# Kernel tuning notes

Measured on AMD Instinct MI355X. Metric: run time of the kernel, lower is better.

## Reference

```python
import jax, jax.numpy as jnp
import numpy as np

N = 50000
E = 800000
F_IN = 128
HID = 128
N_CLS = 32


def setup_inputs() -> dict:
    key = jax.random.key(0)
    ks = jax.random.split(key, 8)
    x = jax.random.normal(ks[0], (N, F_IN), dtype=jnp.float32)
    edge_index = jax.random.randint(ks[1], (2, E), 0, N, dtype=jnp.int32)
    batch = jnp.zeros((N,), dtype=jnp.int32)
    # GCNConv learned params (glorot-ish scale)
    W1 = jax.random.normal(ks[2], (F_IN, HID), dtype=jnp.float32) / np.sqrt(F_IN)
    b1 = jnp.zeros((HID,), dtype=jnp.float32)
    W2 = jax.random.normal(ks[3], (HID, HID), dtype=jnp.float32) / np.sqrt(HID)
    b2 = jnp.zeros((HID,), dtype=jnp.float32)
    W3 = jax.random.normal(ks[4], (HID, N_CLS), dtype=jnp.float32) / np.sqrt(HID)
    b3 = jnp.zeros((N_CLS,), dtype=jnp.float32)
    return {"x": x, "edge_index": edge_index, "batch": batch,
            "W1": W1, "b1": b1, "W2": W2, "b2": b2, "W3": W3, "b3": b3}


def _gcn_norm(edge_index, num_nodes):
    """Add self-loops and compute symmetric D^-1/2 (A+I) D^-1/2 edge weights."""
    loop = jnp.arange(num_nodes, dtype=edge_index.dtype)
    row = jnp.concatenate([edge_index[0], loop])  # source
    col = jnp.concatenate([edge_index[1], loop])  # destination
    ones = jnp.ones(row.shape[0], dtype=jnp.float32)
    deg = jax.ops.segment_sum(ones, col, num_segments=num_nodes)
    dinv = jnp.where(deg > 0, jax.lax.rsqrt(deg), 0.0)
    norm = dinv[row] * dinv[col]  # [E + N]
    return row, col, norm


def _gcn_conv(x, row, col, norm, W, b):
    h = x @ W                               # [N, out]
    msg = h[row] * norm[:, None]            # gather + scale, [E+N, out]
    out = jax.ops.segment_sum(msg, col, num_segments=x.shape[0])
    return out + b


def reference(x, edge_index, batch, W1, b1, W2, b2, W3, b3):
    # eval mode: dropout(p=0.2) is identity
    num_nodes = x.shape[0]
    row, col, norm = _gcn_norm(edge_index, num_nodes)
    h = jax.nn.relu(_gcn_conv(x, row, col, norm, W1, b1))
    h = jax.nn.relu(_gcn_conv(h, row, col, norm, W2, b2))
    out = _gcn_conv(h, row, col, norm, W3, b3)
    return out
```

## Files before the change

kernel.cpp:

```cpp
#include <hip/hip_runtime.h>
#include <math.h>


__global__ __launch_bounds__(256) void count_part_kernel(const int* __restrict__ col,
                                                         int* __restrict__ deg, int E, int n) {
    const int part = blockIdx.x & 7;
    const int nb = gridDim.x >> 3;
    const int chunk = blockIdx.x >> 3;
    const int lo = (int)(((long long)part * n) >> 3);
    const int hi = (int)(((long long)(part + 1) * n) >> 3);
    for (int e = chunk * 256 + threadIdx.x; e < E; e += nb * 256) {
        const int c = col[e];
        if (c >= lo && c < hi) atomicAdd(&deg[c], 1);
    }
}

__global__ __launch_bounds__(256) void scan1_kernel(const int* __restrict__ deg,
                                                    int* __restrict__ local,
                                                    int* __restrict__ blocksums, int n) {
    __shared__ int wsum[4];
    const int t = threadIdx.x;
    const int lane = t & 63;
    const int wv = t >> 6;
    const int base = blockIdx.x * 1024 + t * 4;
    int a0 = (base + 0 < n) ? deg[base + 0] : 0;
    int a1 = (base + 1 < n) ? deg[base + 1] : 0;
    int a2 = (base + 2 < n) ? deg[base + 2] : 0;
    int a3 = (base + 3 < n) ? deg[base + 3] : 0;
    const int tot = a0 + a1 + a2 + a3;
    int incl = tot;
#pragma unroll
    for (int off = 1; off < 64; off <<= 1) {
        int u = __shfl_up(incl, off);
        if (lane >= off) incl += u;
    }
    if (lane == 63) wsum[wv] = incl;
    __syncthreads();
    int woff = 0;
#pragma unroll
    for (int w = 0; w < 4; ++w) woff += (w < wv) ? wsum[w] : 0;
    const int excl = woff + incl - tot;
    if (base + 0 < n) local[base + 0] = excl;
    if (base + 1 < n) local[base + 1] = excl + a0;
    if (base + 2 < n) local[base + 2] = excl + a0 + a1;
    if (base + 3 < n) local[base + 3] = excl + a0 + a1 + a2;
    if (t == 255) blocksums[blockIdx.x] = woff + incl;
}

__global__ void scan2_kernel(const int* __restrict__ blocksums, int* __restrict__ blockoff,
                             int* __restrict__ rowptr, int nb, int n) {
    const int lane = threadIdx.x;
    int v = (lane < nb) ? blocksums[lane] : 0;
    int incl = v;
#pragma unroll
    for (int off = 1; off < 64; off <<= 1) {
        int u = __shfl_up(incl, off);
        if (lane >= off) incl += u;
    }
    if (lane < nb) blockoff[lane] = incl - v;
    if (lane == 63) rowptr[n] = incl;
}

__global__ void scan3_kernel(const int* __restrict__ local, const int* __restrict__ blockoff,
                             const int* __restrict__ deg, int* __restrict__ rowptr,
                             int* __restrict__ cursor, float* __restrict__ dinv, int n) {
    int i = blockIdx.x * blockDim.x + threadIdx.x;
    if (i < n) {
        const int v = local[i] + blockoff[i >> 10];
        rowptr[i] = v;
        cursor[i] = v;
        dinv[i] = rsqrtf((float)deg[i] + 1.0f);
    }
}

__global__ __launch_bounds__(256) void fill_part_kernel(const int* __restrict__ row,
                                                        const int* __restrict__ col,
                                                        int* __restrict__ cursor,
                                                        int* __restrict__ csr, int E, int n) {
    const int part = blockIdx.x & 7;
    const int nb = gridDim.x >> 3;
    const int chunk = blockIdx.x >> 3;
    const int lo = (int)(((long long)part * n) >> 3);
    const int hi = (int)(((long long)(part + 1) * n) >> 3);
    for (int e = chunk * 256 + threadIdx.x; e < E; e += nb * 256) {
        const int c = col[e];
        if (c >= lo && c < hi) {
            const int r = row[e];
            if ((unsigned)r < (unsigned)n) {
                const int pos = atomicAdd(&cursor[c], 1);
                csr[pos] = r;
            }
        }
    }
}

template <int OUT, int COLS, bool CM>
__global__ __launch_bounds__(256) void gemm_kernel(const float* __restrict__ X,
                                                   const float* __restrict__ W,
                                                   const float* __restrict__ dinv,
                                                   float* __restrict__ out, int n) {
    constexpr int NSLAB = OUT / COLS;
    constexpr int CQ  = COLS / 4;
    constexpr int RG  = 256 / CQ;
    constexpr int R   = 4;
    constexpr int RPI = RG * R;
    __shared__ float Wl[128 * COLS];

    const int t = threadIdx.x;
    const int c0 = (int)(blockIdx.x % NSLAB) * COLS;
    const int rowblk = blockIdx.x / NSLAB;

    for (int i = t; i < 128 * CQ; i += 256) {
        const int k  = i / CQ;
        const int cc = i % CQ;
        ((float4*)Wl)[i] = *(const float4*)&W[(size_t)k * OUT + c0 + cc * 4];
    }
    __syncthreads();

    const int cq = t % CQ;
    const int rg = t / CQ;
    const float4* X4 = (const float4*)X;
    const int gcol = c0 + cq * 4;
    const size_t cm_base = (size_t)(gcol >> 4) * n * 16 + (gcol & 15);

    const int r0 = rowblk * RPI + rg * R;
    float4 acc[R];
#pragma unroll
    for (int r = 0; r < R; ++r) acc[r] = make_float4(0.f, 0.f, 0.f, 0.f);

    if (r0 + R <= n) {
#pragma unroll 4
        for (int k4 = 0; k4 < 32; ++k4) {
            const float* wp = &Wl[k4 * 4 * COLS + cq * 4];
            float4 w0 = *(const float4*)(wp);
            float4 w1 = *(const float4*)(wp + COLS);
            float4 w2 = *(const float4*)(wp + 2 * COLS);
            float4 w3 = *(const float4*)(wp + 3 * COLS);
#pragma unroll
            for (int r = 0; r < R; ++r) {
                float4 xv = X4[(size_t)(r0 + r) * 32 + k4];
                acc[r].x = fmaf(xv.x, w0.x, acc[r].x);
                acc[r].x = fmaf(xv.y, w1.x, acc[r].x);
                acc[r].x = fmaf(xv.z, w2.x, acc[r].x);
                acc[r].x = fmaf(xv.w, w3.x, acc[r].x);
                acc[r].y = fmaf(xv.x, w0.y, acc[r].y);
                acc[r].y = fmaf(xv.y, w1.y, acc[r].y);
                acc[r].y = fmaf(xv.z, w2.y, acc[r].y);
                acc[r].y = fmaf(xv.w, w3.y, acc[r].y);
                acc[r].z = fmaf(xv.x, w0.z, acc[r].z);
                acc[r].z = fmaf(xv.y, w1.z, acc[r].z);
                acc[r].z = fmaf(xv.z, w2.z, acc[r].z);
                acc[r].z = fmaf(xv.w, w3.z, acc[r].z);
                acc[r].w = fmaf(xv.x, w0.w, acc[r].w);
                acc[r].w = fmaf(xv.y, w1.w, acc[r].w);
                acc[r].w = fmaf(xv.z, w2.w, acc[r].w);
                acc[r].w = fmaf(xv.w, w3.w, acc[r].w);
            }
        }
#pragma unroll
        for (int r = 0; r < R; ++r) {
            const float s = dinv[r0 + r];
            acc[r].x *= s; acc[r].y *= s; acc[r].z *= s; acc[r].w *= s;
            float* dst = CM ? &out[cm_base + (size_t)(r0 + r) * 16]
                            : &out[(size_t)(r0 + r) * OUT + gcol];
            *(float4*)dst = acc[r];
        }
    } else if (r0 < n) {
        for (int r = 0; r < R; ++r) {
            const int row = r0 + r;
            if (row >= n) break;
            float4 a = make_float4(0.f, 0.f, 0.f, 0.f);
            for (int k4 = 0; k4 < 32; ++k4) {
                float4 xv = X4[(size_t)row * 32 + k4];
                const float* wp = &Wl[k4 * 4 * COLS + cq * 4];
                float4 w0 = *(const float4*)(wp);
                float4 w1 = *(const float4*)(wp + COLS);
                float4 w2 = *(const float4*)(wp + 2 * COLS);
                float4 w3 = *(const float4*)(wp + 3 * COLS);
                a.x = fmaf(xv.x, w0.x, a.x); a.x = fmaf(xv.y, w1.x, a.x);
                a.x = fmaf(xv.z, w2.x, a.x); a.x = fmaf(xv.w, w3.x, a.x);
                a.y = fmaf(xv.x, w0.y, a.y); a.y = fmaf(xv.y, w1.y, a.y);
                a.y = fmaf(xv.z, w2.y, a.y); a.y = fmaf(xv.w, w3.y, a.y);
                a.z = fmaf(xv.x, w0.z, a.z); a.z = fmaf(xv.y, w1.z, a.z);
                a.z = fmaf(xv.z, w2.z, a.z); a.z = fmaf(xv.w, w3.z, a.z);
                a.w = fmaf(xv.x, w0.w, a.w); a.w = fmaf(xv.y, w1.w, a.w);
                a.w = fmaf(xv.z, w2.w, a.w); a.w = fmaf(xv.w, w3.w, a.w);
            }
            const float s = dinv[row];
            a.x *= s; a.y *= s; a.z *= s; a.w *= s;
            float* dst = CM ? &out[cm_base + (size_t)row * 16]
                            : &out[(size_t)row * OUT + gcol];
            *(float4*)dst = a;
        }
    }
}

template <int NC, bool RELU>
__global__ __launch_bounds__(256) void agg_chunk_kernel(const float* __restrict__ hc,
                                                        const int* __restrict__ rowptr,
                                                        const int* __restrict__ csr,
                                                        const float* __restrict__ dinv,
                                                        const float* __restrict__ bias,
                                                        float* __restrict__ out, int n) {
    constexpr int F = NC * 16;
    constexpr int NSPLIT = 8 / NC;
    const int t = threadIdx.x;
    const int slot = blockIdx.x & 7;
    const int cc = slot % NC;
    const int split = slot / NC;
    const int g = (blockIdx.x >> 3) * NSPLIT + split;
    const int node = g * 64 + (t >> 2);
    const int fo = t & 3;
    if (node >= n) return;

    const float4* h4 = (const float4*)(hc + (size_t)cc * n * 16);
    float4 self = h4[(size_t)node * 4 + fo];
    float4 a[8];
#pragma unroll
    for (int j = 0; j < 8; ++j) a[j] = make_float4(0.f, 0.f, 0.f, 0.f);

    const int s = rowptr[node];
    const int e = rowptr[node + 1];
    for (int i = s; i < e; i += 8) {
        int   idx[8];
        float msk[8];
#pragma unroll
        for (int j = 0; j < 8; ++j) {
            const int k = i + j;
            const int kc = (k < e) ? k : (e - 1);
            idx[j] = csr[kc];
            msk[j] = (k < e) ? 1.f : 0.f;
        }
#pragma unroll
        for (int j = 0; j < 8; ++j) {
            float4 v = h4[(size_t)idx[j] * 4 + fo];
            a[j].x = fmaf(v.x, msk[j], a[j].x);
            a[j].y = fmaf(v.y, msk[j], a[j].y);
            a[j].z = fmaf(v.z, msk[j], a[j].z);
            a[j].w = fmaf(v.w, msk[j], a[j].w);
        }
    }
    float accx = self.x + ((a[0].x + a[1].x) + (a[2].x + a[3].x)) + ((a[4].x + a[5].x) + (a[6].x + a[7].x));
    float accy = self.y + ((a[0].y + a[1].y) + (a[2].y + a[3].y)) + ((a[4].y + a[5].y) + (a[6].y + a[7].y));
    float accz = self.z + ((a[0].z + a[1].z) + (a[2].z + a[3].z)) + ((a[4].z + a[5].z) + (a[6].z + a[7].z));
    float accw = self.w + ((a[0].w + a[1].w) + (a[2].w + a[3].w)) + ((a[4].w + a[5].w) + (a[6].w + a[7].w));
    const float dc = dinv[node];
    const int f = cc * 16 + fo * 4;
    const float4 b = *(const float4*)&bias[f];
    float ox = fmaf(accx, dc, b.x);
    float oy = fmaf(accy, dc, b.y);
    float oz = fmaf(accz, dc, b.z);
    float ow = fmaf(accw, dc, b.w);
    if (RELU) {
        ox = fmaxf(ox, 0.f); oy = fmaxf(oy, 0.f);
        oz = fmaxf(oz, 0.f); ow = fmaxf(ow, 0.f);
    }
    float4 res = {ox, oy, oz, ow};
    *(float4*)&out[(size_t)node * F + f] = res;
}

extern "C" void kernel_launch(void* const* d_in, const int* in_sizes, int n_in,
                              void* d_out, int out_size, void* d_ws, size_t ws_size,
                              hipStream_t stream) {
    const float* x  = (const float*)d_in[0];
    const int*   ei = (const int*)d_in[1];
    const float* W1 = (const float*)d_in[3];
    const float* b1 = (const float*)d_in[4];
    const float* W2 = (const float*)d_in[5];
    const float* b2 = (const float*)d_in[6];
    const float* W3 = (const float*)d_in[7];
    const float* b3 = (const float*)d_in[8];
    float* out = (float*)d_out;

    const int N = in_sizes[0] / 128;
    const int E = in_sizes[1] / 2;
    const int* erow = ei;
    const int* ecol = ei + E;

    char* ws = (char*)d_ws;
    auto alloc = [&](size_t bytes) {
        char* p = ws;
        ws += (bytes + 255) & ~(size_t)255;
        return p;
    };
    int*   deg    = (int*)alloc((size_t)N * 4);
    int*   rowptr = (int*)alloc((size_t)(N + 1) * 4);
    int*   cursor = (int*)alloc((size_t)N * 4);
    int*   csr    = (int*)alloc((size_t)E * 4);
    float* dinv   = (float*)alloc((size_t)N * 4);
    float* buf1   = (float*)alloc((size_t)N * 128 * 4);
    float* buf2   = (float*)alloc((size_t)N * 128 * 4);

    int* local = (int*)buf1;
    int* bsums = local + N;
    int* boffs = bsums + 64;

    const int nb = (N + 1023) / 1024;

    hipMemsetAsync(deg, 0, (size_t)N * 4, stream);
    count_part_kernel<<<8 * 128, 256, 0, stream>>>(ecol, deg, E, N);
    scan1_kernel<<<nb, 256, 0, stream>>>(deg, local, bsums, N);
    scan2_kernel<<<1, 64, 0, stream>>>(bsums, boffs, rowptr, nb, N);
    scan3_kernel<<<(N + 255) / 256, 256, 0, stream>>>(local, boffs, deg, rowptr, cursor, dinv, N);
    fill_part_kernel<<<8 * 128, 256, 0, stream>>>(erow, ecol, cursor, csr, E, N);

    const int ngroups = (N + 63) / 64;
    const int g128 = ((N + 63) / 64) * 2;
    const int g32  = (N + 127) / 128;
    const int gagg8 = ngroups * 8;
    const int gagg2 = ((ngroups + 3) / 4) * 8;

    gemm_kernel<128, 64, true><<<g128, 256, 0, stream>>>(x, W1, dinv, buf1, N);
    agg_chunk_kernel<8, true><<<gagg8, 256, 0, stream>>>(buf1, rowptr, csr, dinv, b1, buf2, N);

    gemm_kernel<128, 64, true><<<g128, 256, 0, stream>>>(buf2, W2, dinv, buf1, N);
    agg_chunk_kernel<8, true><<<gagg8, 256, 0, stream>>>(buf1, rowptr, csr, dinv, b2, buf2, N);

    gemm_kernel<32, 32, true><<<g32, 256, 0, stream>>>(buf2, W3, dinv, buf1, N);
    agg_chunk_kernel<2, false><<<gagg2, 256, 0, stream>>>(buf1, rowptr, csr, dinv, b3, out, N);
}
```

Measured before the change: 288.8 us.

## Sort nodes by degree buckets to balance aggregation wavefront work

Adds a counting sort of nodes by in-degree (capped at 63) and has the aggregation kernels process nodes in that order, so threads in a wavefront handle nodes of similar degree and diverge less in the neighbor loop. It adds three small kernels and a memset per call, plus one extra indirection per node. The sorted order scatters the self-feature reads and the output writes, which lowers their coalescing. With uniformly random edges, degrees follow a roughly Poisson distribution around 16, so the balancing gain may be limited.

```diff
diff --git a/kernel.cpp b/kernel.cpp
--- a/kernel.cpp
+++ b/kernel.cpp
@@ -91,6 +91,36 @@
                 csr[pos] = r;
             }
         }
+    }
+}
+
+__global__ void bucket_count_kernel(const int* __restrict__ deg, int* __restrict__ bc, int n) {
+    int i = blockIdx.x * blockDim.x + threadIdx.x;
+    if (i < n) {
+        int b = deg[i]; b = (b < 63) ? b : 63;
+        atomicAdd(&bc[b], 1);
+    }
+}
+
+__global__ void bucket_scan_kernel(const int* __restrict__ bc, int* __restrict__ bcur) {
+    const int lane = threadIdx.x;
+    int v = bc[lane];
+    int incl = v;
+#pragma unroll
+    for (int off = 1; off < 64; off <<= 1) {
+        int u = __shfl_up(incl, off);
+        if (lane >= off) incl += u;
+    }
+    bcur[lane] = incl - v;
+}
+
+__global__ void bucket_scatter_kernel(const int* __restrict__ deg, int* __restrict__ bcur,
+                                      int* __restrict__ order, int n) {
+    int i = blockIdx.x * blockDim.x + threadIdx.x;
+    if (i < n) {
+        int b = deg[i]; b = (b < 63) ? b : 63;
+        const int pos = atomicAdd(&bcur[b], 1);
+        order[pos] = i;
     }
 }
 
@@ -199,6 +229,7 @@
 __global__ __launch_bounds__(256) void agg_chunk_kernel(const float* __restrict__ hc,
                                                         const int* __restrict__ rowptr,
                                                         const int* __restrict__ csr,
+                                                        const int* __restrict__ order,
                                                         const float* __restrict__ dinv,
                                                         const float* __restrict__ bias,
                                                         float* __restrict__ out, int n) {
@@ -209,9 +240,10 @@
     const int cc = slot % NC;
     const int split = slot / NC;
     const int g = (blockIdx.x >> 3) * NSPLIT + split;
-    const int node = g * 64 + (t >> 2);
+    const int idx = g * 64 + (t >> 2);
     const int fo = t & 3;
-    if (node >= n) return;
+    if (idx >= n) return;
+    const int node = order[idx];
 
     const float4* h4 = (const float4*)(hc + (size_t)cc * n * 16);
     float4 self = h4[(size_t)node * 4 + fo];
@@ -222,18 +254,18 @@
     const int s = rowptr[node];
     const int e = rowptr[node + 1];
     for (int i = s; i < e; i += 8) {
-        int   idx[8];
+        int   idxv[8];
         float msk[8];
 #pragma unroll
         for (int j = 0; j < 8; ++j) {
             const int k = i + j;
             const int kc = (k < e) ? k : (e - 1);
-            idx[j] = csr[kc];
+            idxv[j] = csr[kc];
             msk[j] = (k < e) ? 1.f : 0.f;
         }
 #pragma unroll
         for (int j = 0; j < 8; ++j) {
-            float4 v = h4[(size_t)idx[j] * 4 + fo];
+            float4 v = h4[(size_t)idxv[j] * 4 + fo];
             a[j].x = fmaf(v.x, msk[j], a[j].x);
             a[j].y = fmaf(v.y, msk[j], a[j].y);
             a[j].z = fmaf(v.z, msk[j], a[j].z);
@@ -294,6 +326,9 @@
     int* local = (int*)buf1;
     int* bsums = local + N;
     int* boffs = bsums + 64;
+    int* bc    = boffs + 64;
+    int* bcur  = bc + 64;
+    int* order = cursor;
 
     const int nb = (N + 1023) / 1024;
 
@@ -304,6 +339,11 @@
     scan3_kernel<<<(N + 255) / 256, 256, 0, stream>>>(local, boffs, deg, rowptr, cursor, dinv, N);
     fill_part_kernel<<<8 * 128, 256, 0, stream>>>(erow, ecol, cursor, csr, E, N);
 
+    hipMemsetAsync(bc, 0, 64 * 4, stream);
+    bucket_count_kernel<<<(N + 255) / 256, 256, 0, stream>>>(deg, bc, N);
+    bucket_scan_kernel<<<1, 64, 0, stream>>>(bc, bcur);
+    bucket_scatter_kernel<<<(N + 255) / 256, 256, 0, stream>>>(deg, bcur, order, N);
+
     const int ngroups = (N + 63) / 64;
     const int g128 = ((N + 63) / 64) * 2;
     const int g32  = (N + 127) / 128;
@@ -311,11 +351,11 @@
     const int gagg2 = ((ngroups + 3) / 4) * 8;
 
     gemm_kernel<128, 64, true><<<g128, 256, 0, stream>>>(x, W1, dinv, buf1, N);
-    agg_chunk_kernel<8, true><<<gagg8, 256, 0, stream>>>(buf1, rowptr, csr, dinv, b1, buf2, N);
+    agg_chunk_kernel<8, true><<<gagg8, 256, 0, stream>>>(buf1, rowptr, csr, order, dinv, b1, buf2, N);
 
     gemm_kernel<128, 64, true><<<g128, 256, 0, stream>>>(buf2, W2, dinv, buf1, N);
-    agg_chunk_kernel<8, true><<<gagg8, 256, 0, stream>>>(buf1, rowptr, csr, dinv, b2, buf2, N);
+    agg_chunk_kernel<8, true><<<gagg8, 256, 0, stream>>>(buf1, rowptr, csr, order, dinv, b2, buf2, N);
 
     gemm_kernel<32, 32, true><<<g32, 256, 0, stream>>>(buf2, W3, dinv, buf1, N);
-    agg_chunk_kernel<2, false><<<gagg2, 256, 0, stream>>>(buf1, rowptr, csr, dinv, b3, out, N);
-}
+    agg_chunk_kernel<2, false><<<gagg2, 256, 0, stream>>>(buf1, rowptr, csr, order, dinv, b3, out, N);
+}
```

Result: slower. 534.6 us (+85.1%).
